# Kernel optimization log

Hardware: AMD Instinct MI355X
Metric: run time of the kernel (lower is better)

Reference implementation:

```python
import jax, jax.numpy as jnp
import numpy as np

INPUT_DIM = 1024
NUM_HEADS = 16
HEAD_DIM = INPUT_DIM // NUM_HEADS


def setup_inputs() -> dict:
    key = jax.random.key(0)
    ks = jax.random.split(key, 9)
    d = INPUT_DIM
    s = 1.0 / np.sqrt(d)
    x = jax.random.normal(ks[0], (2, 2048, d), dtype=jnp.float32)
    # nn.Linear default init ~ U(-1/sqrt(in), 1/sqrt(in)); weights stored as (out, in), we keep (in, out)
    Wq = jax.random.uniform(ks[1], (d, d), jnp.float32, -s, s)
    bq = jax.random.uniform(ks[2], (d,), jnp.float32, -s, s)
    Wk = jax.random.uniform(ks[3], (d, d), jnp.float32, -s, s)
    bk = jax.random.uniform(ks[4], (d,), jnp.float32, -s, s)
    Wv = jax.random.uniform(ks[5], (d, d), jnp.float32, -s, s)
    bv = jax.random.uniform(ks[6], (d,), jnp.float32, -s, s)
    Wo = jax.random.uniform(ks[7], (d, d), jnp.float32, -s, s)
    bo = jax.random.uniform(ks[8], (d,), jnp.float32, -s, s)
    return {"x": x, "Wq": Wq, "bq": bq, "Wk": Wk, "bk": bk, "Wv": Wv, "bv": bv, "Wo": Wo, "bo": bo}


def reference(x, Wq, bq, Wk, bk, Wv, bv, Wo, bo):
    b, t, d = x.shape
    h, hd = NUM_HEADS, HEAD_DIM
    # projections -> [b, h, t, hd]
    q = (x @ Wq + bq).reshape(b, t, h, hd).transpose(0, 2, 1, 3)
    k = (x @ Wk + bk).reshape(b, t, h, hd).transpose(0, 2, 1, 3)
    v = (x @ Wv + bv).reshape(b, t, h, hd).transpose(0, 2, 1, 3)
    scores = jnp.einsum('bhqd,bhkd->bhqk', q, k) / jnp.sqrt(jnp.float32(hd))
    probs = jax.nn.softmax(scores, axis=-1)
    out = jnp.einsum('bhqk,bhkd->bhqd', probs, v)
    out = out.transpose(0, 2, 1, 3).reshape(b, t, d)
    return out @ Wo + bo
```

## Files before the change

kernel.cpp:

```cpp
#include <hip/hip_runtime.h>
#include <math.h>


#define BATCH 2
#define SEQ   2048
#define DIM   1024
#define NHEAD 16
#define HDIM  64
#define MROWS (BATCH * SEQ)
#define BH    (BATCH * NHEAD)
#define NSPLIT 2
#define TILES_PER_SPLIT (SEQ / 64 / NSPLIT)

typedef __attribute__((ext_vector_type(4))) float     floatx4;
typedef __attribute__((ext_vector_type(4))) float     float4v;
typedef __attribute__((ext_vector_type(8))) _Float16  half8;
typedef __attribute__((ext_vector_type(4))) _Float16  half4;
typedef __attribute__((ext_vector_type(2))) __fp16    fp16x2;

#define SOFT_C 5.77078016f
#define QSCALE 0.18033688f

#if __has_builtin(__builtin_amdgcn_exp2f)
#define EXP2F(x) __builtin_amdgcn_exp2f(x)
#else
#define EXP2F(x) exp2f(x)
#endif

__device__ __forceinline__ void gload16(const void* g, void* l) {
    __builtin_amdgcn_global_load_lds(
        (const __attribute__((address_space(1))) unsigned int*)g,
        (__attribute__((address_space(3))) unsigned int*)l, 16, 0, 0);
}

__device__ __forceinline__ unsigned pk2(float a, float b) {
    fp16x2 v = __builtin_amdgcn_cvt_pkrtz(a, b);
    return __builtin_bit_cast(unsigned, v);
}

__global__ __launch_bounds__(256) void prep(
    const float* __restrict__ x,
    const float* __restrict__ Wq, const float* __restrict__ Wk,
    const float* __restrict__ Wv, const float* __restrict__ Wo,
    _Float16* __restrict__ xh,
    _Float16* __restrict__ Wqt, _Float16* __restrict__ Wkt,
    _Float16* __restrict__ Wvt, _Float16* __restrict__ Wot)
{
    const int tid = threadIdx.x;
    if (blockIdx.z == 4) {
        const int bid = blockIdx.y * 16 + blockIdx.x;
        #pragma unroll
        for (int it = 0; it < 8; ++it) {
            const size_t i = (((size_t)it * 256 + bid) * 256 + tid) * 8;
            float4v a = *(const float4v*)(x + i);
            float4v b = *(const float4v*)(x + i + 4);
            half8 o;
            #pragma unroll
            for (int c = 0; c < 4; ++c) { o[c] = (_Float16)a[c]; o[4+c] = (_Float16)b[c]; }
            *(half8*)(xh + i) = o;
        }
        return;
    }
    __shared__ float tile[64][65];
    const float* W; _Float16* o;
    switch (blockIdx.z) {
        case 0: W = Wq; o = Wqt; break;
        case 1: W = Wk; o = Wkt; break;
        case 2: W = Wv; o = Wvt; break;
        default: W = Wo; o = Wot; break;
    }
    const int n0 = blockIdx.x * 64, k0 = blockIdx.y * 64;
    #pragma unroll
    for (int p = 0; p < 16; ++p) {
        int idx = tid + p * 256;
        int r = idx >> 6, c = idx & 63;
        tile[r][c] = W[(size_t)(k0 + r) * DIM + n0 + c];
    }
    __syncthreads();
    #pragma unroll
    for (int p = 0; p < 16; ++p) {
        int idx = tid + p * 256;
        int r = idx >> 6, c = idx & 63;
        o[(size_t)(n0 + r) * DIM + k0 + c] = (_Float16)tile[c][r];
    }
}

__device__ __forceinline__ void gemm_core16(
    const _Float16* __restrict__ Ap, const _Float16* __restrict__ Bp,
    int m0, int n0, _Float16* AL, _Float16* BL, floatx4 acc[4][4])
{
    const int tid  = threadIdx.x;
    const int wave = tid >> 6;
    const int lane = tid & 63;
    const int li   = lane & 15;
    const int quad = lane >> 4;
    const int wm   = (wave >> 1) * 64;
    const int wn   = (wave & 1) * 64;

    for (int kt = 0; kt < DIM / 64; ++kt) {
        __syncthreads();
        const int k0 = kt * 64;
        #pragma unroll
        for (int p = 0; p < 4; ++p) {
            int s = tid + p * 256;
            int r = s >> 3, ks = s & 7;
            int kg = (ks ^ (r & 7)) << 3;
            int ldsb = (wave * 64 + p * 256) * 8;
            gload16(Ap + (size_t)(m0 + r) * DIM + k0 + kg, AL + ldsb);
            gload16(Bp + (size_t)(n0 + r) * DIM + k0 + kg, BL + ldsb);
        }
        __syncthreads();

        half8 a[4][2], b[4][2];
        #pragma unroll
        for (int i = 0; i < 4; ++i) {
            int ra = (wm + i * 16 + li) << 6;
            int rb = (wn + i * 16 + li) << 6;
            #pragma unroll
            for (int h = 0; h < 2; ++h) {
                a[i][h] = *(const half8*)(AL + ra + (((h * 4 + quad) ^ (li & 7)) << 3));
                b[i][h] = *(const half8*)(BL + rb + (((h * 4 + quad) ^ (li & 7)) << 3));
            }
        }
        #pragma unroll
        for (int i = 0; i < 4; ++i)
            #pragma unroll
            for (int j = 0; j < 4; ++j) {
                acc[i][j] = __builtin_amdgcn_mfma_f32_16x16x32_f16(a[i][0], b[j][0], acc[i][j], 0, 0, 0);
                acc[i][j] = __builtin_amdgcn_mfma_f32_16x16x32_f16(a[i][1], b[j][1], acc[i][j], 0, 0, 0);
            }
    }
}

__global__ __launch_bounds__(256, 2) void qkv_mfma(
    const _Float16* __restrict__ xh,
    const _Float16* __restrict__ Wqt, const _Float16* __restrict__ Wkt,
    const _Float16* __restrict__ Wvt,
    const float* __restrict__ bq, const float* __restrict__ bk,
    const float* __restrict__ bv,
    _Float16* __restrict__ Qh, _Float16* __restrict__ Kh,
    _Float16* __restrict__ Vth)
{
    __shared__ __align__(16) _Float16 SH[128 * 136];
    _Float16* AL = SH;
    _Float16* BL = SH + 128 * 64;

    const int z = blockIdx.z;
    const _Float16* Bp; const float* bias;
    if (z == 0)      { Bp = Wqt; bias = bq; }
    else if (z == 1) { Bp = Wkt; bias = bk; }
    else             { Bp = Wvt; bias = bv; }

    const int m0 = blockIdx.y * 128, n0 = blockIdx.x * 128;

    floatx4 acc[4][4];
    #pragma unroll
    for (int i = 0; i < 4; ++i)
        #pragma unroll
        for (int j = 0; j < 4; ++j) acc[i][j] = (floatx4){0.f, 0.f, 0.f, 0.f};

    gemm_core16(xh, Bp, m0, n0, AL, BL, acc);

    const int tid = threadIdx.x, wave = tid >> 6, lane = tid & 63;
    const int li = lane & 15, quad = lane >> 4;
    const int wm = (wave >> 1) * 64, wn = (wave & 1) * 64;
    const int bb = m0 >> 11, t0 = m0 & 2047;

    if (z != 2) {
        _Float16* out = (z == 0) ? Qh : Kh;
        const float sc = (z == 0) ? QSCALE : 1.0f;
        #pragma unroll
        for (int i = 0; i < 4; ++i)
            #pragma unroll
            for (int j = 0; j < 4; ++j) {
                int n = n0 + wn + j * 16 + li;
                int h = n >> 6, hd = n & 63;
                float b_ = bias[n];
                #pragma unroll
                for (int r = 0; r < 4; ++r) {
                    int m = m0 + wm + i * 16 + quad * 4 + r;
                    int t = m & 2047;
                    out[(((size_t)(bb * NHEAD + h) * SEQ) + t) * HDIM + hd] =
                        (_Float16)((acc[i][j][r] + b_) * sc);
                }
            }
    } else {
        __syncthreads();
        #pragma unroll
        for (int i = 0; i < 4; ++i)
            #pragma unroll
            for (int j = 0; j < 4; ++j) {
                int n = wn + j * 16 + li;
                float b_ = bias[n0 + n];
                half4 w;
                #pragma unroll
                for (int r = 0; r < 4; ++r) w[r] = (_Float16)(acc[i][j][r] + b_);
                *(half4*)(SH + n * 136 + wm + i * 16 + quad * 4) = w;
            }
        __syncthreads();
        #pragma unroll
        for (int p = 0; p < 8; ++p) {
            int idx = p * 256 + tid;
            int v = idx >> 4, c8 = (idx & 15) * 8;
            half8 w = *(const half8*)(SH + v * 136 + c8);
            int n = n0 + v;
            int h = n >> 6, hd = n & 63;
            *(half8*)(Vth + ((size_t)(bb * NHEAD + h) * HDIM + hd) * SEQ + t0 + c8) = w;
        }
    }
}

#define LDP 72

__global__ __launch_bounds__(256) void attn(
    const _Float16* __restrict__ Q, const _Float16* __restrict__ K,
    const _Float16* __restrict__ Vt,
    _Float16* __restrict__ Op0, _Float16* __restrict__ Op1,
    float* __restrict__ rsb)
{
    __shared__ __align__(16) _Float16 Ks[64 * 64];
    __shared__ __align__(16) _Float16 Vs[64 * 64];
    __shared__ __align__(16) _Float16 Pt[4][32 * LDP];

    const int tid  = threadIdx.x;
    const int wave = tid >> 6;
    const int lane = tid & 63;
    const int li   = lane & 15;
    const int quad = lane >> 4;
    const int bh   = blockIdx.y;
    const int q0   = blockIdx.x * 128;
    const int z    = blockIdx.z;
    const int b    = bh >> 4, h = bh & 15;

    half8 qa[2][2];
    #pragma unroll
    for (int nq = 0; nq < 2; ++nq) {
        size_t qrow = ((size_t)bh * SEQ + q0 + wave * 32 + nq * 16 + li) * HDIM;
        qa[nq][0] = *(const half8*)(Q + qrow + quad * 8);
        qa[nq][1] = *(const half8*)(Q + qrow + 32 + quad * 8);
    }

    half8 onesA;
    {
        _Float16 v = (li == 0) ? (_Float16)1.0f : (_Float16)0.0f;
        #pragma unroll
        for (int c = 0; c < 8; ++c) onesA[c] = v;
    }

    floatx4 O[4][2];
    floatx4 rsacc[2];
    #pragma unroll
    for (int nq = 0; nq < 2; ++nq) {
        rsacc[nq] = (floatx4){0.f, 0.f, 0.f, 0.f};
        #pragma unroll
        for (int i = 0; i < 4; ++i) O[i][nq] = (floatx4){0.f, 0.f, 0.f, 0.f};
    }

    const _Float16* Kbh = K  + (size_t)bh * SEQ * HDIM;
    const _Float16* Vbh = Vt + (size_t)bh * HDIM * SEQ;
    _Float16* Pw = Pt[wave];

    for (int kt = z * TILES_PER_SPLIT; kt < (z + 1) * TILES_PER_SPLIT; ++kt) {
        __syncthreads();
        {
            const _Float16* Kg = Kbh + (size_t)kt * 64 * HDIM;
            const _Float16* Vg = Vbh + kt * 64;
            #pragma unroll
            for (int p = 0; p < 2; ++p) {
                int s = tid + p * 256;
                int r = s >> 3, ks = s & 7;
                int kg = (ks ^ (r & 7)) << 3;
                int ldsb = (wave * 64 + p * 256) * 8;
                gload16(Kg + r * HDIM + kg, (_Float16*)Ks + ldsb);
                gload16(Vg + (size_t)r * SEQ + kg, (_Float16*)Vs + ldsb);
            }
        }
        __syncthreads();

        #pragma unroll
        for (int mb = 0; mb < 4; ++mb) {
            int row = (mb * 16 + li) << 6;
            half8 a0 = *(const half8*)(Ks + row + ((quad ^ (li & 7)) << 3));
            half8 a1 = *(const half8*)(Ks + row + (((quad + 4) ^ (li & 7)) << 3));
            #pragma unroll
            for (int nq = 0; nq < 2; ++nq) {
                floatx4 st = (floatx4){0.f, 0.f, 0.f, 0.f};
                st = __builtin_amdgcn_mfma_f32_16x16x32_f16(a0, qa[nq][0], st, 0, 0, 0);
                st = __builtin_amdgcn_mfma_f32_16x16x32_f16(a1, qa[nq][1], st, 0, 0, 0);
                float p0 = EXP2F(st[0] - SOFT_C);
                float p1 = EXP2F(st[1] - SOFT_C);
                float p2 = EXP2F(st[2] - SOFT_C);
                float p3 = EXP2F(st[3] - SOFT_C);
                uint2 w; w.x = pk2(p0, p1); w.y = pk2(p2, p3);
                *(uint2*)(Pw + (nq * 16 + li) * LDP + mb * 16 + quad * 4) = w;
            }
        }

        half8 pb[2][2];
        #pragma unroll
        for (int nq = 0; nq < 2; ++nq) {
            pb[nq][0] = *(const half8*)(Pw + (nq * 16 + li) * LDP + quad * 8);
            pb[nq][1] = *(const half8*)(Pw + (nq * 16 + li) * LDP + 32 + quad * 8);
        }
        #pragma unroll
        for (int nq = 0; nq < 2; ++nq) {
            rsacc[nq] = __builtin_amdgcn_mfma_f32_16x16x32_f16(onesA, pb[nq][0], rsacc[nq], 0, 0, 0);
            rsacc[nq] = __builtin_amdgcn_mfma_f32_16x16x32_f16(onesA, pb[nq][1], rsacc[nq], 0, 0, 0);
        }
        #pragma unroll
        for (int mb = 0; mb < 4; ++mb) {
            int row = (mb * 16 + li) << 6;
            half8 v0 = *(const half8*)(Vs + row + ((quad ^ (li & 7)) << 3));
            half8 v1 = *(const half8*)(Vs + row + (((quad + 4) ^ (li & 7)) << 3));
            #pragma unroll
            for (int nq = 0; nq < 2; ++nq) {
                O[mb][nq] = __builtin_amdgcn_mfma_f32_16x16x32_f16(v0, pb[nq][0], O[mb][nq], 0, 0, 0);
                O[mb][nq] = __builtin_amdgcn_mfma_f32_16x16x32_f16(v1, pb[nq][1], O[mb][nq], 0, 0, 0);
            }
        }
    }

    if (quad == 0) {
        #pragma unroll
        for (int nq = 0; nq < 2; ++nq)
            rsb[((size_t)z * BH + bh) * SEQ + q0 + wave * 32 + nq * 16 + li] = rsacc[nq][0];
    }

    _Float16* Op = (z == 0) ? Op0 : Op1;

    #pragma unroll
    for (int mb = 0; mb < 4; ++mb)
        #pragma unroll
        for (int nq = 0; nq < 2; ++nq) {
            uint2 w;
            w.x = pk2(O[mb][nq][0], O[mb][nq][1]);
            w.y = pk2(O[mb][nq][2], O[mb][nq][3]);
            *(uint2*)(Pw + (nq * 16 + li) * LDP + mb * 16 + quad * 4) = w;
        }
    #pragma unroll
    for (int p = 0; p < 4; ++p) {
        int idx = p * 64 + lane;
        int qq = idx >> 3, c8 = (idx & 7) * 8;
        half8 v = *(const half8*)(Pw + qq * LDP + c8);
        size_t row = (size_t)b * SEQ + q0 + wave * 32 + qq;
        *(half8*)(Op + row * DIM + h * HDIM + c8) = v;
    }
}

__global__ __launch_bounds__(256) void combine(
    const _Float16* __restrict__ Op0, const _Float16* __restrict__ Op1,
    const float* __restrict__ rsb, _Float16* __restrict__ Ctx)
{
    const size_t idx8 = (size_t)blockIdx.x * 256 + threadIdx.x;
    const int m = (int)(idx8 >> 7);
    const int c = (int)(idx8 & 127);
    const int h = c >> 3;
    const int b = m >> 11, t = m & 2047;
    const size_t rsi = (size_t)(b * NHEAD + h) * SEQ + t;
    const float r0 = rsb[rsi];
    const float r1 = rsb[(size_t)BH * SEQ + rsi];
    const float inv = 1.0f / (r0 + r1);
    const size_t off = idx8 * 8;
    half8 o0 = *(const half8*)(Op0 + off);
    half8 o1 = *(const half8*)(Op1 + off);
    half8 o;
    #pragma unroll
    for (int r = 0; r < 8; ++r)
        o[r] = (_Float16)(((float)o0[r] + (float)o1[r]) * inv);
    *(half8*)(Ctx + off) = o;
}

__global__ __launch_bounds__(256, 2) void out_mfma(
    const _Float16* __restrict__ Ctx, const _Float16* __restrict__ Wot,
    const float* __restrict__ bo, float* __restrict__ out)
{
    __shared__ __align__(16) _Float16 AL[128 * 64];
    __shared__ __align__(16) _Float16 BL[128 * 64];

    const int m0 = blockIdx.y * 128, n0 = blockIdx.x * 128;

    floatx4 acc[4][4];
    #pragma unroll
    for (int i = 0; i < 4; ++i)
        #pragma unroll
        for (int j = 0; j < 4; ++j) acc[i][j] = (floatx4){0.f, 0.f, 0.f, 0.f};

    gemm_core16(Ctx, Wot, m0, n0, AL, BL, acc);

    const int tid = threadIdx.x, wave = tid >> 6, lane = tid & 63;
    const int li = lane & 15, quad = lane >> 4;
    const int wm = (wave >> 1) * 64, wn = (wave & 1) * 64;

    #pragma unroll
    for (int i = 0; i < 4; ++i)
        #pragma unroll
        for (int j = 0; j < 4; ++j) {
            int n = n0 + wn + j * 16 + li;
            float b_ = bo[n];
            #pragma unroll
            for (int r = 0; r < 4; ++r) {
                int m = m0 + wm + i * 16 + quad * 4 + r;
                out[(size_t)m * DIM + n] = acc[i][j][r] + b_;
            }
        }
}

extern "C" void kernel_launch(void* const* d_in, const int* in_sizes, int n_in,
                              void* d_out, int out_size, void* d_ws, size_t ws_size,
                              hipStream_t stream) {
    const float* x  = (const float*)d_in[0];
    const float* Wq = (const float*)d_in[1];
    const float* bq = (const float*)d_in[2];
    const float* Wk = (const float*)d_in[3];
    const float* bk = (const float*)d_in[4];
    const float* Wv = (const float*)d_in[5];
    const float* bv = (const float*)d_in[6];
    const float* Wo = (const float*)d_in[7];
    const float* bo = (const float*)d_in[8];
    float* out = (float*)d_out;

    const size_t PX = (size_t)MROWS * DIM;
    const size_t PW = (size_t)DIM * DIM;
    _Float16* xh  = (_Float16*)d_ws;
    _Float16* Wqt = xh + PX;
    _Float16* Wkt = Wqt + PW;
    _Float16* Wvt = Wkt + PW;
    _Float16* Wot = Wvt + PW;
    _Float16* Qh  = Wot + PW;
    _Float16* Kh  = Qh + PX;
    _Float16* Op1 = Kh + PX;
    _Float16* Vth = Op1 + PX;

    _Float16* Op0 = xh;
    float*    rsb = (float*)Wqt;
    _Float16* Ctx = xh;

    prep<<<dim3(16, 16, 5), 256, 0, stream>>>(
        x, Wq, Wk, Wv, Wo, xh, Wqt, Wkt, Wvt, Wot);

    qkv_mfma<<<dim3(DIM / 128, MROWS / 128, 3), 256, 0, stream>>>(
        xh, Wqt, Wkt, Wvt, bq, bk, bv, Qh, Kh, Vth);

    attn<<<dim3(SEQ / 128, BH, NSPLIT), 256, 0, stream>>>(
        Qh, Kh, Vth, Op0, Op1, rsb);

    combine<<<dim3(PX / 8 / 256), 256, 0, stream>>>(Op0, Op1, rsb, Ctx);

    out_mfma<<<dim3(DIM / 128, MROWS / 128), 256, 0, stream>>>(
        Ctx, Wot, bo, out);
}
```

Baseline: 198.7 us.

## Double-buffer K/V tiles and keep P in registers via permlane swaps

The attention kernel now double-buffers the K/V LDS tiles, so the async global-to-LDS loads for the next tile are issued before computing the current one, and only one barrier is needed per iteration. The probability matrix is no longer round-tripped through LDS. It is reshuffled into MFMA B-operand layout in registers using permlane32/permlane16 swaps. The softmax offset is folded into the accumulator's initial value, and the output staging reuses the K buffer with an XOR swizzle. The risks are more LDS per block (32KB), a correctness dependence on the permlane layout mapping, and whether the async loads are actually waited for before the barrier.

```diff
diff --git a/kernel.cpp b/kernel.cpp
--- a/kernel.cpp
+++ b/kernel.cpp
@@ -17,6 +17,7 @@
 typedef __attribute__((ext_vector_type(8))) _Float16  half8;
 typedef __attribute__((ext_vector_type(4))) _Float16  half4;
 typedef __attribute__((ext_vector_type(2))) __fp16    fp16x2;
+typedef __attribute__((ext_vector_type(4))) unsigned  uint4v;
 
 #define SOFT_C 5.77078016f
 #define QSCALE 0.18033688f
@@ -36,6 +37,21 @@
 __device__ __forceinline__ unsigned pk2(float a, float b) {
     fp16x2 v = __builtin_amdgcn_cvt_pkrtz(a, b);
     return __builtin_bit_cast(unsigned, v);
+}
+
+__device__ __forceinline__ void plswap(unsigned &a, unsigned &b) {
+#if __has_builtin(__builtin_amdgcn_permlane32_swap) && __has_builtin(__builtin_amdgcn_permlane16_swap)
+    auto r32 = __builtin_amdgcn_permlane32_swap(a, b, false, false);
+    auto r16 = __builtin_amdgcn_permlane16_swap(r32[0], r32[1], false, false);
+    a = r16[0]; b = r16[1];
+#else
+    asm volatile("s_nop 1\n\t"
+                 "v_permlane32_swap_b32 %0, %1\n\t"
+                 "s_nop 1\n\t"
+                 "v_permlane16_swap_b32 %0, %1\n\t"
+                 "s_nop 1"
+                 : "+v"(a), "+v"(b));
+#endif
 }
 
 __global__ __launch_bounds__(256) void prep(
@@ -210,17 +226,14 @@
     }
 }
 
-#define LDP 72
-
-__global__ __launch_bounds__(256) void attn(
+__global__ __launch_bounds__(256, 4) void attn(
     const _Float16* __restrict__ Q, const _Float16* __restrict__ K,
     const _Float16* __restrict__ Vt,
     _Float16* __restrict__ Op0, _Float16* __restrict__ Op1,
     float* __restrict__ rsb)
 {
-    __shared__ __align__(16) _Float16 Ks[64 * 64];
-    __shared__ __align__(16) _Float16 Vs[64 * 64];
-    __shared__ __align__(16) _Float16 Pt[4][32 * LDP];
+    __shared__ __align__(16) _Float16 Ks[2][64 * 64];
+    __shared__ __align__(16) _Float16 Vs[2][64 * 64];
 
     const int tid  = threadIdx.x;
     const int wave = tid >> 6;
@@ -258,50 +271,70 @@
 
     const _Float16* Kbh = K  + (size_t)bh * SEQ * HDIM;
     const _Float16* Vbh = Vt + (size_t)bh * HDIM * SEQ;
-    _Float16* Pw = Pt[wave];
-
-    for (int kt = z * TILES_PER_SPLIT; kt < (z + 1) * TILES_PER_SPLIT; ++kt) {
-        __syncthreads();
-        {
-            const _Float16* Kg = Kbh + (size_t)kt * 64 * HDIM;
-            const _Float16* Vg = Vbh + kt * 64;
-            #pragma unroll
-            for (int p = 0; p < 2; ++p) {
-                int s = tid + p * 256;
-                int r = s >> 3, ks = s & 7;
-                int kg = (ks ^ (r & 7)) << 3;
-                int ldsb = (wave * 64 + p * 256) * 8;
-                gload16(Kg + r * HDIM + kg, (_Float16*)Ks + ldsb);
-                gload16(Vg + (size_t)r * SEQ + kg, (_Float16*)Vs + ldsb);
-            }
-        }
-        __syncthreads();
-
+
+    const int kt0 = z * TILES_PER_SPLIT, kt1 = kt0 + TILES_PER_SPLIT;
+
+    auto stage = [&](int buf, int kt_) {
+        const _Float16* Kg = Kbh + (size_t)kt_ * 64 * HDIM;
+        const _Float16* Vg = Vbh + kt_ * 64;
+        _Float16* Kl = &Ks[buf][0];
+        _Float16* Vl = &Vs[buf][0];
+        #pragma unroll
+        for (int p = 0; p < 2; ++p) {
+            int s = tid + p * 256;
+            int r = s >> 3, ks = s & 7;
+            int kg = (ks ^ (r & 7)) << 3;
+            int ldsb = (wave * 64 + p * 256) * 8;
+            gload16(Kg + r * HDIM + kg, Kl + ldsb);
+            gload16(Vg + (size_t)r * SEQ + kg, Vl + ldsb);
+        }
+    };
+
+    stage(0, kt0);
+    __syncthreads();
+    int cur = 0;
+
+    for (int kt = kt0; kt < kt1; ++kt) {
+        if (kt + 1 < kt1) stage(cur ^ 1, kt + 1);
+        const _Float16* Kc = &Ks[cur][0];
+        const _Float16* Vc = &Vs[cur][0];
+
+        unsigned R[2][4][2];
         #pragma unroll
         for (int mb = 0; mb < 4; ++mb) {
             int row = (mb * 16 + li) << 6;
-            half8 a0 = *(const half8*)(Ks + row + ((quad ^ (li & 7)) << 3));
-            half8 a1 = *(const half8*)(Ks + row + (((quad + 4) ^ (li & 7)) << 3));
+            half8 a0 = *(const half8*)(Kc + row + ((quad ^ (li & 7)) << 3));
+            half8 a1 = *(const half8*)(Kc + row + (((quad + 4) ^ (li & 7)) << 3));
             #pragma unroll
             for (int nq = 0; nq < 2; ++nq) {
-                floatx4 st = (floatx4){0.f, 0.f, 0.f, 0.f};
+                floatx4 st = (floatx4){-SOFT_C, -SOFT_C, -SOFT_C, -SOFT_C};
                 st = __builtin_amdgcn_mfma_f32_16x16x32_f16(a0, qa[nq][0], st, 0, 0, 0);
                 st = __builtin_amdgcn_mfma_f32_16x16x32_f16(a1, qa[nq][1], st, 0, 0, 0);
-                float p0 = EXP2F(st[0] - SOFT_C);
-                float p1 = EXP2F(st[1] - SOFT_C);
-                float p2 = EXP2F(st[2] - SOFT_C);
-                float p3 = EXP2F(st[3] - SOFT_C);
-                uint2 w; w.x = pk2(p0, p1); w.y = pk2(p2, p3);
-                *(uint2*)(Pw + (nq * 16 + li) * LDP + mb * 16 + quad * 4) = w;
+                R[nq][mb][0] = pk2(EXP2F(st[0]), EXP2F(st[1]));
+                R[nq][mb][1] = pk2(EXP2F(st[2]), EXP2F(st[3]));
             }
         }
 
         half8 pb[2][2];
         #pragma unroll
-        for (int nq = 0; nq < 2; ++nq) {
-            pb[nq][0] = *(const half8*)(Pw + (nq * 16 + li) * LDP + quad * 8);
-            pb[nq][1] = *(const half8*)(Pw + (nq * 16 + li) * LDP + 32 + quad * 8);
-        }
+        for (int nq = 0; nq < 2; ++nq)
+            #pragma unroll
+            for (int f = 0; f < 2; ++f) {
+                unsigned w0, w1, w2, w3;
+                {
+                    unsigned x = R[nq][2 * f][0], y = R[nq][2 * f + 1][0];
+                    plswap(x, y);
+                    w0 = x; w2 = y;
+                }
+                {
+                    unsigned x = R[nq][2 * f][1], y = R[nq][2 * f + 1][1];
+                    plswap(x, y);
+                    w1 = x; w3 = y;
+                }
+                uint4v uw; uw[0] = w0; uw[1] = w1; uw[2] = w2; uw[3] = w3;
+                pb[nq][f] = __builtin_bit_cast(half8, uw);
+            }
+
         #pragma unroll
         for (int nq = 0; nq < 2; ++nq) {
             rsacc[nq] = __builtin_amdgcn_mfma_f32_16x16x32_f16(onesA, pb[nq][0], rsacc[nq], 0, 0, 0);
@@ -310,14 +343,17 @@
         #pragma unroll
         for (int mb = 0; mb < 4; ++mb) {
             int row = (mb * 16 + li) << 6;
-            half8 v0 = *(const half8*)(Vs + row + ((quad ^ (li & 7)) << 3));
-            half8 v1 = *(const half8*)(Vs + row + (((quad + 4) ^ (li & 7)) << 3));
+            half8 v0 = *(const half8*)(Vc + row + ((quad ^ (li & 7)) << 3));
+            half8 v1 = *(const half8*)(Vc + row + (((quad + 4) ^ (li & 7)) << 3));
             #pragma unroll
             for (int nq = 0; nq < 2; ++nq) {
                 O[mb][nq] = __builtin_amdgcn_mfma_f32_16x16x32_f16(v0, pb[nq][0], O[mb][nq], 0, 0, 0);
                 O[mb][nq] = __builtin_amdgcn_mfma_f32_16x16x32_f16(v1, pb[nq][1], O[mb][nq], 0, 0, 0);
             }
         }
+
+        __syncthreads();
+        cur ^= 1;
     }
 
     if (quad == 0) {
@@ -328,6 +364,7 @@
 
     _Float16* Op = (z == 0) ? Op0 : Op1;
 
+    _Float16* Sw = &Ks[0][0] + wave * (32 * 64);
     #pragma unroll
     for (int mb = 0; mb < 4; ++mb)
         #pragma unroll
@@ -335,15 +372,18 @@
             uint2 w;
             w.x = pk2(O[mb][nq][0], O[mb][nq][1]);
             w.y = pk2(O[mb][nq][2], O[mb][nq][3]);
-            *(uint2*)(Pw + (nq * 16 + li) * LDP + mb * 16 + quad * 4) = w;
+            int row = nq * 16 + li;
+            int col = mb * 16 + quad * 4;
+            int swc = (((col >> 3) ^ (row & 7)) << 3) | (col & 7);
+            *(uint2*)(Sw + row * 64 + swc) = w;
         }
     #pragma unroll
     for (int p = 0; p < 4; ++p) {
         int idx = p * 64 + lane;
-        int qq = idx >> 3, c8 = (idx & 7) * 8;
-        half8 v = *(const half8*)(Pw + qq * LDP + c8);
+        int qq = idx >> 3, c = idx & 7;
+        half8 v = *(const half8*)(Sw + qq * 64 + ((c ^ (qq & 7)) << 3));
         size_t row = (size_t)b * SEQ + q0 + wave * 32 + qq;
-        *(half8*)(Op + row * DIM + h * HDIM + c8) = v;
+        *(half8*)(Op + row * DIM + h * HDIM + c * 8) = v;
     }
 }
 
```

Result: faster. 185.6 us (-6.6%).
